# Kernel tuning notes

Hardware: AMD Instinct MI355X
Metric: run time of the kernel (lower is better)

Reference implementation:

```python
import jax, jax.numpy as jnp
import numpy as np

B, N, DIM = 4, 16384, 512
H, D, S = 8, 64, 64  # heads, dim_head, n_global_queries
SCALE = 1.0  # FLARE hardcodes scale=1.0


def setup_inputs() -> dict:
    key = jax.random.key(0)
    ks = jax.random.split(key, 10)
    inner = H * D
    s = 0.02
    return {
        "x": jax.random.normal(ks[0], (B, N, DIM), dtype=jnp.float32),
        "q_global": jax.random.normal(ks[1], (1, H, S, D), dtype=jnp.float32),
        "Wx": jax.random.normal(ks[2], (DIM, inner), dtype=jnp.float32) * s,
        "bx": jnp.zeros((inner,), dtype=jnp.float32),
        "Wk": jax.random.normal(ks[3], (D, D), dtype=jnp.float32) * s,
        "bk": jnp.zeros((D,), dtype=jnp.float32),
        "Wv": jax.random.normal(ks[4], (D, D), dtype=jnp.float32) * s,
        "bv": jnp.zeros((D,), dtype=jnp.float32),
        "Wo": jax.random.normal(ks[5], (inner, DIM), dtype=jnp.float32) * s,
        "bo": jnp.zeros((DIM,), dtype=jnp.float32),
    }


def reference(x, q_global, Wx, bx, Wk, bk, Wv, bv, Wo, bo):
    b, n, c = x.shape
    # input projection + split heads: B N (H D) -> B H N D
    x_mid = (x @ Wx + bx).reshape(b, n, H, D).transpose(0, 2, 1, 3)
    # per-head k/v projections (dim_head x dim_head)
    k = x_mid @ Wk + bk  # [B,H,N,D]
    v = x_mid @ Wv + bv  # [B,H,N,D]
    G = q_global  # broadcast over batch
    # pass 1: aggregate tokens into S global slots
    attn1 = jax.nn.softmax(jnp.einsum('bhsd,bhnd->bhsn', jnp.broadcast_to(G, (b, H, S, D)), k) * SCALE, axis=-1)
    z = jnp.einsum('bhsn,bhnd->bhsd', attn1, v)  # [B,H,S,D]
    # pass 2: distribute slots back to tokens (query=k, key=G, value=z)
    attn2 = jax.nn.softmax(jnp.einsum('bhnd,bhsd->bhns', k, jnp.broadcast_to(G, (b, H, S, D))) * SCALE, axis=-1)
    y = jnp.einsum('bhns,bhsd->bhnd', attn2, z)  # [B,H,N,D]
    # merge heads + output projection
    out = y.transpose(0, 2, 1, 3).reshape(b, n, H * D)
    return out @ Wo + bo
```

## Files before the change

kernel.cpp:

```cpp
#include <hip/hip_runtime.h>
#include <stdint.h>

#define DEV __device__ __forceinline__

typedef __attribute__((ext_vector_type(8))) short bf16x8;
typedef __attribute__((ext_vector_type(4))) float f32x4;
typedef __attribute__((ext_vector_type(8))) unsigned short u16x8;
typedef __attribute__((ext_vector_type(4))) unsigned short u16x4;

DEV unsigned short f2bf(float f) {
  union { float f; unsigned int u; } v; v.f = f;
  unsigned int u = v.u;
  return (unsigned short)((u + 0x7FFFu + ((u >> 16) & 1u)) >> 16);
}

DEV f32x4 mfma16(bf16x8 a, bf16x8 b, f32x4 c) {
  return __builtin_amdgcn_mfma_f32_16x16x32_bf16(a, b, c, 0, 0, 0);
}

DEV void gl_lds16(const void* g, void* l) {
  __builtin_amdgcn_global_load_lds(
      (const __attribute__((address_space(1))) void*)g,
      (__attribute__((address_space(3))) void*)l, 16, 0, 0);
}

__global__ __launch_bounds__(256) void k_cvt_bf16(const float* __restrict__ in,
                                                  unsigned short* __restrict__ out,
                                                  int n8) {
  int i = blockIdx.x * 256 + threadIdx.x;
  if (i >= n8) return;
  const float4* p = (const float4*)in + (size_t)i * 2;
  float4 a = p[0], b = p[1];
  u16x8 o;
  o[0] = f2bf(a.x); o[1] = f2bf(a.y); o[2] = f2bf(a.z); o[3] = f2bf(a.w);
  o[4] = f2bf(b.x); o[5] = f2bf(b.y); o[6] = f2bf(b.z); o[7] = f2bf(b.w);
  ((u16x8*)out)[i] = o;
}

__global__ __launch_bounds__(256) void k_fuse_wkv(const float* __restrict__ Wx,
                                                  const float* __restrict__ Wk,
                                                  const float* __restrict__ Wv,
                                                  unsigned short* __restrict__ WkvT) {
  int idx = blockIdx.x * 256 + threadIdx.x;
  int o = idx >> 9;
  int c = idx & 511;
  const float* W = (o < 512) ? Wk : Wv;
  int oo = o & 511;
  int hb = oo & ~63;
  int dp = oo & 63;
  float s = 0.f;
#pragma unroll 8
  for (int d = 0; d < 64; ++d) s += Wx[(size_t)c * 512 + hb + d] * W[d * 64 + dp];
  WkvT[(size_t)o * 512 + c] = f2bf(s);
}

__global__ void k_fuse_bias(const float* __restrict__ bx, const float* __restrict__ bk,
                            const float* __restrict__ bv, const float* __restrict__ Wk,
                            const float* __restrict__ Wv, float* __restrict__ bkv) {
  int o = blockIdx.x * 256 + threadIdx.x;
  if (o >= 1024) return;
  const float* W = (o < 512) ? Wk : Wv;
  const float* bb = (o < 512) ? bk : bv;
  int oo = o & 511, hb = oo & ~63, dp = oo & 63;
  float s = bb[dp];
  for (int d = 0; d < 64; ++d) s += bx[hb + d] * W[d * 64 + dp];
  bkv[o] = s;
}

__global__ void k_wo_t(const float* __restrict__ Wo, unsigned short* __restrict__ WoT) {
  int idx = blockIdx.x * 256 + threadIdx.x;
  int i = idx >> 9, o = idx & 511;
  WoT[(size_t)o * 512 + i] = f2bf(Wo[(size_t)i * 512 + o]);
}

template <int MODE>
__global__ __launch_bounds__(256) void k_gemm(const unsigned short* __restrict__ A,
                                              const unsigned short* __restrict__ BT,
                                              const float* __restrict__ bias,
                                              void* __restrict__ Cptr,
                                              unsigned short* __restrict__ vT, int NT) {
  __shared__ unsigned short As[2][128 * 64];
  __shared__ unsigned short Bs[2][128 * 64];
  const int tid = threadIdx.x;
  const int w = tid >> 6, lane = tid & 63;
  const int l = lane & 15, g = lane >> 4;
  unsigned bid = blockIdx.x;
  unsigned perx = gridDim.x >> 3;
  unsigned nbid = (bid & 7) * perx + (bid >> 3);
  const int ntile = nbid % NT, mtile = nbid / NT;
  const int bm = mtile * 128, bn = ntile * 128;
  const int wm = (w >> 1) * 64, wn = (w & 1) * 64;
  const int lr = lane >> 3;
  const int lc = (lane & 7) * 8;
  f32x4 acc[4][4] = {};

#define STAGE(buf, k0)                                                        \
  {                                                                           \
    _Pragma("unroll") for (int i = 0; i < 4; ++i) {                           \
      int q = w * 4 + i;                                                      \
      int row = q * 8 + lr;                                                   \
      gl_lds16(A + (size_t)(bm + row) * 512 + (k0) + lc, &As[buf][q * 512]);  \
      gl_lds16(BT + (size_t)(bn + row) * 512 + (k0) + lc, &Bs[buf][q * 512]); \
    }                                                                         \
  }

  STAGE(0, 0);
  __syncthreads();
  int cur = 0;
#pragma unroll 2
  for (int t = 0; t < 8; ++t) {
    if (t < 7) STAGE(cur ^ 1, (t + 1) * 64);
#pragma unroll
    for (int ks = 0; ks < 2; ++ks) {
      bf16x8 af[4], bfr[4];
#pragma unroll
      for (int fm = 0; fm < 4; ++fm)
        af[fm] = *(const bf16x8*)&As[cur][(wm + fm * 16 + l) * 64 + ks * 32 + g * 8];
#pragma unroll
      for (int fn = 0; fn < 4; ++fn)
        bfr[fn] = *(const bf16x8*)&Bs[cur][(wn + fn * 16 + l) * 64 + ks * 32 + g * 8];
#pragma unroll
      for (int fm = 0; fm < 4; ++fm)
#pragma unroll
        for (int fn = 0; fn < 4; ++fn)
          acc[fm][fn] = mfma16(af[fm], bfr[fn], acc[fm][fn]);
    }
    __syncthreads();
    cur ^= 1;
  }
#undef STAGE

#pragma unroll
  for (int fm = 0; fm < 4; ++fm)
#pragma unroll
    for (int fn = 0; fn < 4; ++fn) {
      int colg = bn + wn + fn * 16 + l;
      float bcol = bias[colg];
      int row0 = bm + wm + fm * 16 + g * 4;
      if (MODE == 0) {
#pragma unroll
        for (int r = 0; r < 4; ++r)
          ((float*)Cptr)[(size_t)(row0 + r) * 512 + colg] = acc[fm][fn][r] + bcol;
      } else {
        if (colg < 512) {
#pragma unroll
          for (int r = 0; r < 4; ++r)
            ((unsigned short*)Cptr)[(size_t)(row0 + r) * 512 + colg] =
                f2bf(acc[fm][fn][r] + bcol);
        } else {
          int c2 = colg - 512, h = c2 >> 6, d = c2 & 63;
          int b = row0 >> 14, nn = row0 & 16383;
          u16x4 o;
#pragma unroll
          for (int r = 0; r < 4; ++r) o[r] = f2bf(acc[fm][fn][r] + bcol);
          *(u16x4*)&vT[(((size_t)(b * 8 + h)) * 64 + d) * 16384 + nn] = o;
        }
      }
    }
}

__global__ __launch_bounds__(256) void k_pass1(const unsigned short* __restrict__ kb,
                                               const unsigned short* __restrict__ vT,
                                               const float* __restrict__ qg,
                                               float* __restrict__ zpart,
                                               float* __restrict__ mpart,
                                               float* __restrict__ dpart) {
  __shared__ unsigned short Gs[64 * 72];
  __shared__ unsigned short Ks[128 * 72];
  __shared__ unsigned short Vs[64 * 136];
  __shared__ unsigned short Ps[64 * 136];
  int chunk = blockIdx.x, bh = blockIdx.y;
  int b = bh >> 3, h = bh & 7;
  int tid = threadIdx.x, w = tid >> 6, lane = tid & 63, l = lane & 15, g = lane >> 4;
  {
    int s = tid >> 2, dc = (tid & 3) * 16;
    const float* src = qg + ((size_t)h * 64 + s) * 64 + dc;
    u16x8 o0, o1;
#pragma unroll
    for (int e = 0; e < 8; ++e) { o0[e] = f2bf(src[e]); o1[e] = f2bf(src[8 + e]); }
    *(u16x8*)&Gs[s * 72 + dc] = o0;
    *(u16x8*)&Gs[s * 72 + dc + 8] = o1;
  }
  f32x4 zacc[4] = {};
  float m_run = -1e30f, d_run = 0.f;
  int n_base = chunk * 1024;
  for (int t = 0; t < 8; ++t) {
    int n0 = n_base + t * 128;
#pragma unroll
    for (int i = 0; i < 4; ++i) {
      int cc = i * 256 + tid;
      int nl = cc >> 3, dc = (cc & 7) * 8;
      *(u16x8*)&Ks[nl * 72 + dc] =
          *(const u16x8*)&kb[((size_t)(b * 16384 + n0 + nl)) * 512 + h * 64 + dc];
    }
#pragma unroll
    for (int i = 0; i < 4; ++i) {
      int cc = i * 256 + tid;
      int d = cc >> 4, nc = (cc & 15) * 8;
      *(u16x8*)&Vs[d * 136 + nc] =
          *(const u16x8*)&vT[((size_t)(bh * 64 + d)) * 16384 + n0 + nc];
    }
    __syncthreads();
    f32x4 sacc[8] = {};
#pragma unroll
    for (int ks = 0; ks < 2; ++ks) {
      bf16x8 bq = *(const bf16x8*)&Gs[(w * 16 + l) * 72 + ks * 32 + g * 8];
#pragma unroll
      for (int fm = 0; fm < 8; ++fm) {
        bf16x8 ak = *(const bf16x8*)&Ks[(fm * 16 + l) * 72 + ks * 32 + g * 8];
        sacc[fm] = mfma16(ak, bq, sacc[fm]);
      }
    }
    float tmax = -1e30f;
#pragma unroll
    for (int fm = 0; fm < 8; ++fm)
#pragma unroll
      for (int r = 0; r < 4; ++r) tmax = fmaxf(tmax, sacc[fm][r]);
    tmax = fmaxf(tmax, __shfl_xor(tmax, 16));
    tmax = fmaxf(tmax, __shfl_xor(tmax, 32));
    float newm = fmaxf(m_run, tmax);
    float scale = __expf(m_run - newm);
    float psum = 0.f;
#pragma unroll
    for (int fm = 0; fm < 8; ++fm) {
      u16x4 pp;
#pragma unroll
      for (int r = 0; r < 4; ++r) {
        float p = __expf(sacc[fm][r] - newm);
        psum += p;
        pp[r] = f2bf(p);
      }
      *(u16x4*)&Ps[(w * 16 + l) * 136 + fm * 16 + g * 4] = pp;
    }
    psum += __shfl_xor(psum, 16);
    psum += __shfl_xor(psum, 32);
    d_run = d_run * scale + psum;
    m_run = newm;
    float sc[4];
#pragma unroll
    for (int r = 0; r < 4; ++r) sc[r] = __shfl(scale, g * 4 + r);
#pragma unroll
    for (int fd = 0; fd < 4; ++fd)
#pragma unroll
      for (int r = 0; r < 4; ++r) zacc[fd][r] *= sc[r];
#pragma unroll
    for (int kc = 0; kc < 4; ++kc) {
      bf16x8 ap = *(const bf16x8*)&Ps[(w * 16 + l) * 136 + kc * 32 + g * 8];
#pragma unroll
      for (int fd = 0; fd < 4; ++fd) {
        bf16x8 bv = *(const bf16x8*)&Vs[(fd * 16 + l) * 136 + kc * 32 + g * 8];
        zacc[fd] = mfma16(ap, bv, zacc[fd]);
      }
    }
    __syncthreads();
  }
  size_t base = ((size_t)bh * 16 + chunk) * 64;
#pragma unroll
  for (int fd = 0; fd < 4; ++fd)
#pragma unroll
    for (int r = 0; r < 4; ++r) {
      int s = w * 16 + g * 4 + r, d = fd * 16 + l;
      zpart[(base + s) * 64 + d] = zacc[fd][r];
    }
  if (g == 0) {
    mpart[base + w * 16 + l] = m_run;
    dpart[base + w * 16 + l] = d_run;
  }
}

__global__ void k_zred(const float* __restrict__ zpart, const float* __restrict__ mpart,
                       const float* __restrict__ dpart, unsigned short* __restrict__ zT) {
  int bh = blockIdx.x, tid = threadIdx.x;
  for (int i = 0; i < 16; ++i) {
    int idx = i * 256 + tid;
    int s = idx >> 6, d = idx & 63;
    float mg = -1e30f;
    for (int c = 0; c < 16; ++c) mg = fmaxf(mg, mpart[((size_t)bh * 16 + c) * 64 + s]);
    float den = 0.f, num = 0.f;
    for (int c = 0; c < 16; ++c) {
      float e = __expf(mpart[((size_t)bh * 16 + c) * 64 + s] - mg);
      den += e * dpart[((size_t)bh * 16 + c) * 64 + s];
      num += e * zpart[(((size_t)bh * 16 + c) * 64 + s) * 64 + d];
    }
    zT[((size_t)bh * 64 + d) * 64 + s] = f2bf(num / den);
  }
}

__global__ __launch_bounds__(256) void k_pass2(const unsigned short* __restrict__ kb,
                                               const unsigned short* __restrict__ zT,
                                               const float* __restrict__ qg,
                                               unsigned short* __restrict__ y) {
  __shared__ unsigned short Gs[64 * 72];
  __shared__ unsigned short Zs[64 * 72];
  __shared__ unsigned short P2s[4][32 * 72];
  int tc = blockIdx.x, bh = blockIdx.y, b = bh >> 3, h = bh & 7;
  int tid = threadIdx.x, w = tid >> 6, lane = tid & 63, l = lane & 15, g = lane >> 4;
  {
    int s = tid >> 2, dc = (tid & 3) * 16;
    const float* src = qg + ((size_t)h * 64 + s) * 64 + dc;
    u16x8 o0, o1;
#pragma unroll
    for (int e = 0; e < 8; ++e) { o0[e] = f2bf(src[e]); o1[e] = f2bf(src[8 + e]); }
    *(u16x8*)&Gs[s * 72 + dc] = o0;
    *(u16x8*)&Gs[s * 72 + dc + 8] = o1;
#pragma unroll
    for (int j = 0; j < 2; ++j) {
      int cc = j * 256 + tid;
      int d2 = cc >> 3, sc8 = (cc & 7) * 8;
      *(u16x8*)&Zs[d2 * 72 + sc8] = *(const u16x8*)&zT[((size_t)bh * 64 + d2) * 64 + sc8];
    }
  }
  __syncthreads();
  for (int it = 0; it < 4; ++it) {
    int tok0 = tc * 512 + w * 128 + it * 32;
    bf16x8 ak[2][2];
#pragma unroll
    for (int fm = 0; fm < 2; ++fm)
#pragma unroll
      for (int ks = 0; ks < 2; ++ks)
        ak[fm][ks] = *(const bf16x8*)&kb[((size_t)(b * 16384) + tok0 + fm * 16 + l) * 512 +
                                         h * 64 + ks * 32 + g * 8];
    f32x4 sacc[2][4] = {};
#pragma unroll
    for (int ks = 0; ks < 2; ++ks)
#pragma unroll
      for (int fs = 0; fs < 4; ++fs) {
        bf16x8 bq = *(const bf16x8*)&Gs[(fs * 16 + l) * 72 + ks * 32 + g * 8];
#pragma unroll
        for (int fm = 0; fm < 2; ++fm) sacc[fm][fs] = mfma16(ak[fm][ks], bq, sacc[fm][fs]);
      }
    float inv_[2][4];
#pragma unroll
    for (int fm = 0; fm < 2; ++fm) {
      float mx[4];
#pragma unroll
      for (int r = 0; r < 4; ++r) {
        float m4 = fmaxf(fmaxf(sacc[fm][0][r], sacc[fm][1][r]),
                         fmaxf(sacc[fm][2][r], sacc[fm][3][r]));
#pragma unroll
        for (int msk = 1; msk < 16; msk <<= 1) m4 = fmaxf(m4, __shfl_xor(m4, msk));
        mx[r] = m4;
      }
#pragma unroll
      for (int r = 0; r < 4; ++r) {
        float s4 = 0.f;
#pragma unroll
        for (int fs = 0; fs < 4; ++fs) {
          float p = __expf(sacc[fm][fs][r] - mx[r]);
          sacc[fm][fs][r] = p;
          s4 += p;
        }
#pragma unroll
        for (int msk = 1; msk < 16; msk <<= 1) s4 += __shfl_xor(s4, msk);
        inv_[fm][r] = 1.f / s4;
      }
#pragma unroll
      for (int fs = 0; fs < 4; ++fs)
#pragma unroll
        for (int r = 0; r < 4; ++r)
          P2s[w][(fm * 16 + g * 4 + r) * 72 + fs * 16 + l] = f2bf(sacc[fm][fs][r]);
    }
    f32x4 yacc[2][4] = {};
#pragma unroll
    for (int kc = 0; kc < 2; ++kc) {
      bf16x8 aP[2];
#pragma unroll
      for (int fm = 0; fm < 2; ++fm)
        aP[fm] = *(const bf16x8*)&P2s[w][(fm * 16 + l) * 72 + kc * 32 + g * 8];
#pragma unroll
      for (int fd = 0; fd < 4; ++fd) {
        bf16x8 bz = *(const bf16x8*)&Zs[(fd * 16 + l) * 72 + kc * 32 + g * 8];
#pragma unroll
        for (int fm = 0; fm < 2; ++fm) yacc[fm][fd] = mfma16(aP[fm], bz, yacc[fm][fd]);
      }
    }
#pragma unroll
    for (int fm = 0; fm < 2; ++fm)
#pragma unroll
      for (int fd = 0; fd < 4; ++fd)
#pragma unroll
        for (int r = 0; r < 4; ++r) {
          int tok = tok0 + fm * 16 + g * 4 + r;
          y[((size_t)(b * 16384) + tok) * 512 + h * 64 + fd * 16 + l] =
              f2bf(yacc[fm][fd][r] * inv_[fm][r]);
        }
  }
}

extern "C" void kernel_launch(void* const* d_in, const int* in_sizes, int n_in,
                              void* d_out, int out_size, void* d_ws, size_t ws_size,
                              hipStream_t stream) {
  const float* x  = (const float*)d_in[0];
  const float* qg = (const float*)d_in[1];
  const float* Wx = (const float*)d_in[2];
  const float* bx = (const float*)d_in[3];
  const float* Wk = (const float*)d_in[4];
  const float* bk = (const float*)d_in[5];
  const float* Wv = (const float*)d_in[6];
  const float* bv = (const float*)d_in[7];
  const float* Wo = (const float*)d_in[8];
  const float* bo = (const float*)d_in[9];
  float* out = (float*)d_out;

  char* ws = (char*)d_ws;
  unsigned short* xbf  = (unsigned short*)(ws);
  unsigned short* vT   = (unsigned short*)(ws + 67108864);
  unsigned short* WkvT = (unsigned short*)(ws + 134217728);
  unsigned short* WoT  = (unsigned short*)(ws + 135266304);
  float* bkv           = (float*)(ws + 135790592);
  float* zpart         = (float*)(ws + 135794688);
  float* mpart         = (float*)(ws + 144183296);
  float* dpart         = (float*)(ws + 144314368);
  unsigned short* zT   = (unsigned short*)(ws + 144445440);
  unsigned short* kbuf = (unsigned short*)d_out;

  k_cvt_bf16<<<dim3(16384), dim3(256), 0, stream>>>(x, xbf, 4194304);
  k_fuse_wkv<<<dim3(2048), dim3(256), 0, stream>>>(Wx, Wk, Wv, WkvT);
  k_fuse_bias<<<dim3(4), dim3(256), 0, stream>>>(bx, bk, bv, Wk, Wv, bkv);
  k_wo_t<<<dim3(1024), dim3(256), 0, stream>>>(Wo, WoT);
  k_gemm<1><<<dim3(4096), dim3(256), 0, stream>>>(xbf, WkvT, bkv, (void*)kbuf, vT, 8);
  k_pass1<<<dim3(16, 32), dim3(256), 0, stream>>>(kbuf, vT, qg, zpart, mpart, dpart);
  k_zred<<<dim3(32), dim3(256), 0, stream>>>(zpart, mpart, dpart, zT);
  k_pass2<<<dim3(32, 32), dim3(256), 0, stream>>>(kbuf, zT, qg, xbf);
  k_gemm<0><<<dim3(2048), dim3(256), 0, stream>>>(xbf, WoT, bo, (void*)out, nullptr, 4);
}
```

Measured before the change: 327.3 us.

## Fold global queries into projection weights and fold z into output projection

Precomputes Wx·Wk·Gᵀ so the first GEMM emits attention logits L directly instead of k, which removes the QK matmuls from both passes. Pass 2 and the output projection merge into one GEMM: a per-row softmax of L times a per-batch z·Wo matrix. The first GEMM's K-tile shrinks from 64 to 32, and pass1 now reads V straight from global memory rather than staging it in LDS. In exchange it adds several small precompute kernels, rounds the logits to bf16, and writes a per-batch zWoT matrix.

```diff
diff --git a/kernel.cpp b/kernel.cpp
--- a/kernel.cpp
+++ b/kernel.cpp
@@ -13,11 +13,13 @@
   unsigned int u = v.u;
   return (unsigned short)((u + 0x7FFFu + ((u >> 16) & 1u)) >> 16);
 }
-
+DEV float bf2f(unsigned short u) {
+  union { unsigned int u; float f; } v; v.u = ((unsigned int)u) << 16;
+  return v.f;
+}
 DEV f32x4 mfma16(bf16x8 a, bf16x8 b, f32x4 c) {
   return __builtin_amdgcn_mfma_f32_16x16x32_bf16(a, b, c, 0, 0, 0);
 }
-
 DEV void gl_lds16(const void* g, void* l) {
   __builtin_amdgcn_global_load_lds(
       (const __attribute__((address_space(1))) void*)g,
@@ -37,34 +39,59 @@
   ((u16x8*)out)[i] = o;
 }
 
-__global__ __launch_bounds__(256) void k_fuse_wkv(const float* __restrict__ Wx,
-                                                  const float* __restrict__ Wk,
-                                                  const float* __restrict__ Wv,
-                                                  unsigned short* __restrict__ WkvT) {
+__global__ void k_gk(const float* __restrict__ Wk, const float* __restrict__ qg,
+                     float* __restrict__ GK) {
   int idx = blockIdx.x * 256 + threadIdx.x;
-  int o = idx >> 9;
-  int c = idx & 511;
-  const float* W = (o < 512) ? Wk : Wv;
-  int oo = o & 511;
-  int hb = oo & ~63;
-  int dp = oo & 63;
-  float s = 0.f;
+  int dd = idx & 63, s = (idx >> 6) & 63, h = idx >> 12;
+  float a = 0.f;
 #pragma unroll 8
-  for (int d = 0; d < 64; ++d) s += Wx[(size_t)c * 512 + hb + d] * W[d * 64 + dp];
-  WkvT[(size_t)o * 512 + c] = f2bf(s);
-}
-
-__global__ void k_fuse_bias(const float* __restrict__ bx, const float* __restrict__ bk,
-                            const float* __restrict__ bv, const float* __restrict__ Wk,
-                            const float* __restrict__ Wv, float* __restrict__ bkv) {
+  for (int d = 0; d < 64; ++d) a += Wk[dd * 64 + d] * qg[((size_t)(h * 64 + s)) * 64 + d];
+  GK[idx] = a;
+}
+
+__global__ void k_wl(const float* __restrict__ Wx, const float* __restrict__ GK,
+                     unsigned short* __restrict__ Wcat) {
+  int idx = blockIdx.x * 256 + threadIdx.x;
+  int c = idx & 511, hs = idx >> 9;
+  int h = hs >> 6;
+  float a = 0.f;
+#pragma unroll 8
+  for (int dd = 0; dd < 64; ++dd) a += Wx[(size_t)c * 512 + h * 64 + dd] * GK[hs * 64 + dd];
+  Wcat[(size_t)hs * 512 + c] = f2bf(a);
+}
+
+__global__ void k_wv(const float* __restrict__ Wx, const float* __restrict__ Wv,
+                     unsigned short* __restrict__ Wcat) {
+  int idx = blockIdx.x * 256 + threadIdx.x;
+  int c = idx & 511, o = idx >> 9;
+  int h = o >> 6, dp = o & 63;
+  float a = 0.f;
+#pragma unroll 8
+  for (int dd = 0; dd < 64; ++dd) a += Wx[(size_t)c * 512 + h * 64 + dd] * Wv[dd * 64 + dp];
+  Wcat[(size_t)(512 + o) * 512 + c] = f2bf(a);
+}
+
+__global__ void k_bias(const float* __restrict__ bx, const float* __restrict__ bk,
+                       const float* __restrict__ bv, const float* __restrict__ Wk,
+                       const float* __restrict__ Wv, const float* __restrict__ qg,
+                       float* __restrict__ bias) {
   int o = blockIdx.x * 256 + threadIdx.x;
   if (o >= 1024) return;
-  const float* W = (o < 512) ? Wk : Wv;
-  const float* bb = (o < 512) ? bk : bv;
-  int oo = o & 511, hb = oo & ~63, dp = oo & 63;
-  float s = bb[dp];
-  for (int d = 0; d < 64; ++d) s += bx[hb + d] * W[d * 64 + dp];
-  bkv[o] = s;
+  if (o < 512) {
+    int h = o >> 6, s = o & 63;
+    float a = 0.f;
+    for (int dp = 0; dp < 64; ++dp) {
+      float bkf = bk[dp];
+      for (int dd = 0; dd < 64; ++dd) bkf += bx[h * 64 + dd] * Wk[dd * 64 + dp];
+      a += bkf * qg[((size_t)(h * 64 + s)) * 64 + dp];
+    }
+    bias[o] = a;
+  } else {
+    int o2 = o - 512, h = o2 >> 6, dp = o2 & 63;
+    float a = bv[dp];
+    for (int dd = 0; dd < 64; ++dd) a += bx[h * 64 + dd] * Wv[dd * 64 + dp];
+    bias[o] = a;
+  }
 }
 
 __global__ void k_wo_t(const float* __restrict__ Wo, unsigned short* __restrict__ WoT) {
@@ -73,14 +100,13 @@
   WoT[(size_t)o * 512 + i] = f2bf(Wo[(size_t)i * 512 + o]);
 }
 
-template <int MODE>
-__global__ __launch_bounds__(256) void k_gemm(const unsigned short* __restrict__ A,
-                                              const unsigned short* __restrict__ BT,
-                                              const float* __restrict__ bias,
-                                              void* __restrict__ Cptr,
-                                              unsigned short* __restrict__ vT, int NT) {
-  __shared__ unsigned short As[2][128 * 64];
-  __shared__ unsigned short Bs[2][128 * 64];
+__global__ __launch_bounds__(256) void k_gemm1(const unsigned short* __restrict__ A,
+                                               const unsigned short* __restrict__ BT,
+                                               const float* __restrict__ bias,
+                                               unsigned short* __restrict__ Lout,
+                                               unsigned short* __restrict__ vT, int NT) {
+  __shared__ unsigned short As[2][4096];
+  __shared__ unsigned short Bs[2][4096];
   const int tid = threadIdx.x;
   const int w = tid >> 6, lane = tid & 63;
   const int l = lane & 15, g = lane >> 4;
@@ -90,45 +116,42 @@
   const int ntile = nbid % NT, mtile = nbid / NT;
   const int bm = mtile * 128, bn = ntile * 128;
   const int wm = (w >> 1) * 64, wn = (w & 1) * 64;
-  const int lr = lane >> 3;
-  const int lc = (lane & 7) * 8;
+  const int lr = lane >> 2;
+  const int lc = (lane & 3) * 8;
   f32x4 acc[4][4] = {};
 
-#define STAGE(buf, k0)                                                        \
+#define STG(buf, k0)                                                          \
   {                                                                           \
-    _Pragma("unroll") for (int i = 0; i < 4; ++i) {                           \
-      int q = w * 4 + i;                                                      \
-      int row = q * 8 + lr;                                                   \
+    _Pragma("unroll") for (int i = 0; i < 2; ++i) {                           \
+      int q = w * 2 + i;                                                      \
+      int row = q * 16 + lr;                                                  \
       gl_lds16(A + (size_t)(bm + row) * 512 + (k0) + lc, &As[buf][q * 512]);  \
       gl_lds16(BT + (size_t)(bn + row) * 512 + (k0) + lc, &Bs[buf][q * 512]); \
     }                                                                         \
   }
 
-  STAGE(0, 0);
+  STG(0, 0);
   __syncthreads();
   int cur = 0;
 #pragma unroll 2
-  for (int t = 0; t < 8; ++t) {
-    if (t < 7) STAGE(cur ^ 1, (t + 1) * 64);
-#pragma unroll
-    for (int ks = 0; ks < 2; ++ks) {
-      bf16x8 af[4], bfr[4];
-#pragma unroll
-      for (int fm = 0; fm < 4; ++fm)
-        af[fm] = *(const bf16x8*)&As[cur][(wm + fm * 16 + l) * 64 + ks * 32 + g * 8];
+  for (int t = 0; t < 16; ++t) {
+    if (t < 15) STG(cur ^ 1, (t + 1) * 32);
+    bf16x8 af[4], bfr[4];
+#pragma unroll
+    for (int fm = 0; fm < 4; ++fm)
+      af[fm] = *(const bf16x8*)&As[cur][(wm + fm * 16 + l) * 32 + g * 8];
+#pragma unroll
+    for (int fn = 0; fn < 4; ++fn)
+      bfr[fn] = *(const bf16x8*)&Bs[cur][(wn + fn * 16 + l) * 32 + g * 8];
+#pragma unroll
+    for (int fm = 0; fm < 4; ++fm)
 #pragma unroll
       for (int fn = 0; fn < 4; ++fn)
-        bfr[fn] = *(const bf16x8*)&Bs[cur][(wn + fn * 16 + l) * 64 + ks * 32 + g * 8];
-#pragma unroll
-      for (int fm = 0; fm < 4; ++fm)
-#pragma unroll
-        for (int fn = 0; fn < 4; ++fn)
-          acc[fm][fn] = mfma16(af[fm], bfr[fn], acc[fm][fn]);
-    }
+        acc[fm][fn] = mfma16(af[fm], bfr[fn], acc[fm][fn]);
     __syncthreads();
     cur ^= 1;
   }
-#undef STAGE
+#undef STG
 
 #pragma unroll
   for (int fm = 0; fm < 4; ++fm)
@@ -137,101 +160,74 @@
       int colg = bn + wn + fn * 16 + l;
       float bcol = bias[colg];
       int row0 = bm + wm + fm * 16 + g * 4;
-      if (MODE == 0) {
+      if (colg < 512) {
 #pragma unroll
         for (int r = 0; r < 4; ++r)
-          ((float*)Cptr)[(size_t)(row0 + r) * 512 + colg] = acc[fm][fn][r] + bcol;
+          Lout[(size_t)(row0 + r) * 512 + colg] = f2bf(acc[fm][fn][r] + bcol);
       } else {
-        if (colg < 512) {
-#pragma unroll
-          for (int r = 0; r < 4; ++r)
-            ((unsigned short*)Cptr)[(size_t)(row0 + r) * 512 + colg] =
-                f2bf(acc[fm][fn][r] + bcol);
-        } else {
-          int c2 = colg - 512, h = c2 >> 6, d = c2 & 63;
-          int b = row0 >> 14, nn = row0 & 16383;
-          u16x4 o;
-#pragma unroll
-          for (int r = 0; r < 4; ++r) o[r] = f2bf(acc[fm][fn][r] + bcol);
-          *(u16x4*)&vT[(((size_t)(b * 8 + h)) * 64 + d) * 16384 + nn] = o;
-        }
-      }
-    }
-}
-
-__global__ __launch_bounds__(256) void k_pass1(const unsigned short* __restrict__ kb,
+        int c2 = colg - 512, h = c2 >> 6, d = c2 & 63;
+        int b = row0 >> 14, nn = row0 & 16383;
+        u16x4 o;
+#pragma unroll
+        for (int r = 0; r < 4; ++r) o[r] = f2bf(acc[fm][fn][r] + bcol);
+        *(u16x4*)&vT[(((size_t)(b * 8 + h)) * 64 + d) * 16384 + nn] = o;
+      }
+    }
+}
+
+__global__ __launch_bounds__(256) void k_pass1(const unsigned short* __restrict__ L,
                                                const unsigned short* __restrict__ vT,
-                                               const float* __restrict__ qg,
                                                float* __restrict__ zpart,
                                                float* __restrict__ mpart,
                                                float* __restrict__ dpart) {
-  __shared__ unsigned short Gs[64 * 72];
-  __shared__ unsigned short Ks[128 * 72];
-  __shared__ unsigned short Vs[64 * 136];
-  __shared__ unsigned short Ps[64 * 136];
+  __shared__ unsigned short Ls[64 * 128];
   int chunk = blockIdx.x, bh = blockIdx.y;
   int b = bh >> 3, h = bh & 7;
   int tid = threadIdx.x, w = tid >> 6, lane = tid & 63, l = lane & 15, g = lane >> 4;
-  {
-    int s = tid >> 2, dc = (tid & 3) * 16;
-    const float* src = qg + ((size_t)h * 64 + s) * 64 + dc;
-    u16x8 o0, o1;
-#pragma unroll
-    for (int e = 0; e < 8; ++e) { o0[e] = f2bf(src[e]); o1[e] = f2bf(src[8 + e]); }
-    *(u16x8*)&Gs[s * 72 + dc] = o0;
-    *(u16x8*)&Gs[s * 72 + dc + 8] = o1;
-  }
+  const int sn = tid & 127, sg = tid >> 7;
   f32x4 zacc[4] = {};
   float m_run = -1e30f, d_run = 0.f;
-  int n_base = chunk * 1024;
+  const int s = w * 16 + l;
   for (int t = 0; t < 8; ++t) {
-    int n0 = n_base + t * 128;
-#pragma unroll
-    for (int i = 0; i < 4; ++i) {
-      int cc = i * 256 + tid;
-      int nl = cc >> 3, dc = (cc & 7) * 8;
-      *(u16x8*)&Ks[nl * 72 + dc] =
-          *(const u16x8*)&kb[((size_t)(b * 16384 + n0 + nl)) * 512 + h * 64 + dc];
-    }
-#pragma unroll
-    for (int i = 0; i < 4; ++i) {
-      int cc = i * 256 + tid;
-      int d = cc >> 4, nc = (cc & 15) * 8;
-      *(u16x8*)&Vs[d * 136 + nc] =
-          *(const u16x8*)&vT[((size_t)(bh * 64 + d)) * 16384 + n0 + nc];
+    int n0 = chunk * 1024 + t * 128;
+    if (t) __syncthreads();
+#pragma unroll
+    for (int j = 0; j < 4; ++j) {
+      int s0 = sg * 32 + j * 8;
+      u16x8 vl = *(const u16x8*)&L[((size_t)(b * 16384 + n0 + sn)) * 512 + h * 64 + s0];
+#pragma unroll
+      for (int e = 0; e < 8; ++e) {
+        int ss = s0 + e;
+        Ls[(ss * 256 + ((sn * 2) ^ ((ss & 7) << 4))) >> 1] = vl[e];
+      }
     }
     __syncthreads();
-    f32x4 sacc[8] = {};
-#pragma unroll
-    for (int ks = 0; ks < 2; ++ks) {
-      bf16x8 bq = *(const bf16x8*)&Gs[(w * 16 + l) * 72 + ks * 32 + g * 8];
-#pragma unroll
-      for (int fm = 0; fm < 8; ++fm) {
-        bf16x8 ak = *(const bf16x8*)&Ks[(fm * 16 + l) * 72 + ks * 32 + g * 8];
-        sacc[fm] = mfma16(ak, bq, sacc[fm]);
-      }
-    }
+    bf16x8 aL[4];
+#pragma unroll
+    for (int kc = 0; kc < 4; ++kc)
+      aL[kc] = *(const bf16x8*)&Ls[(s * 256 + ((kc * 64 + g * 16) ^ ((s & 7) << 4))) >> 1];
+    float fv[32];
+#pragma unroll
+    for (int kc = 0; kc < 4; ++kc)
+#pragma unroll
+      for (int e = 0; e < 8; ++e) fv[kc * 8 + e] = bf2f((unsigned short)aL[kc][e]);
     float tmax = -1e30f;
 #pragma unroll
-    for (int fm = 0; fm < 8; ++fm)
-#pragma unroll
-      for (int r = 0; r < 4; ++r) tmax = fmaxf(tmax, sacc[fm][r]);
+    for (int i = 0; i < 32; ++i) tmax = fmaxf(tmax, fv[i]);
     tmax = fmaxf(tmax, __shfl_xor(tmax, 16));
     tmax = fmaxf(tmax, __shfl_xor(tmax, 32));
     float newm = fmaxf(m_run, tmax);
     float scale = __expf(m_run - newm);
     float psum = 0.f;
-#pragma unroll
-    for (int fm = 0; fm < 8; ++fm) {
-      u16x4 pp;
-#pragma unroll
-      for (int r = 0; r < 4; ++r) {
-        float p = __expf(sacc[fm][r] - newm);
+    bf16x8 pf[4];
+#pragma unroll
+    for (int kc = 0; kc < 4; ++kc)
+#pragma unroll
+      for (int e = 0; e < 8; ++e) {
+        float p = __expf(fv[kc * 8 + e] - newm);
         psum += p;
-        pp[r] = f2bf(p);
-      }
-      *(u16x4*)&Ps[(w * 16 + l) * 136 + fm * 16 + g * 4] = pp;
-    }
+        pf[kc][e] = (short)f2bf(p);
+      }
     psum += __shfl_xor(psum, 16);
     psum += __shfl_xor(psum, 32);
     d_run = d_run * scale + psum;
@@ -245,22 +241,21 @@
       for (int r = 0; r < 4; ++r) zacc[fd][r] *= sc[r];
 #pragma unroll
     for (int kc = 0; kc < 4; ++kc) {
-      bf16x8 ap = *(const bf16x8*)&Ps[(w * 16 + l) * 136 + kc * 32 + g * 8];
 #pragma unroll
       for (int fd = 0; fd < 4; ++fd) {
-        bf16x8 bv = *(const bf16x8*)&Vs[(fd * 16 + l) * 136 + kc * 32 + g * 8];
-        zacc[fd] = mfma16(ap, bv, zacc[fd]);
-      }
-    }
-    __syncthreads();
+        bf16x8 bv = *(const bf16x8*)&vT[((size_t)(bh * 64 + fd * 16 + l)) * 16384 + n0 +
+                                        kc * 32 + g * 8];
+        zacc[fd] = mfma16(pf[kc], bv, zacc[fd]);
+      }
+    }
   }
   size_t base = ((size_t)bh * 16 + chunk) * 64;
 #pragma unroll
   for (int fd = 0; fd < 4; ++fd)
 #pragma unroll
     for (int r = 0; r < 4; ++r) {
-      int s = w * 16 + g * 4 + r, d = fd * 16 + l;
-      zpart[(base + s) * 64 + d] = zacc[fd][r];
+      int so = w * 16 + g * 4 + r, d = fd * 16 + l;
+      zpart[(base + so) * 64 + d] = zacc[fd][r];
     }
   if (g == 0) {
     mpart[base + w * 16 + l] = m_run;
@@ -269,7 +264,7 @@
 }
 
 __global__ void k_zred(const float* __restrict__ zpart, const float* __restrict__ mpart,
-                       const float* __restrict__ dpart, unsigned short* __restrict__ zT) {
+                       const float* __restrict__ dpart, float* __restrict__ z) {
   int bh = blockIdx.x, tid = threadIdx.x;
   for (int i = 0; i < 16; ++i) {
     int idx = i * 256 + tid;
@@ -282,108 +277,94 @@
       den += e * dpart[((size_t)bh * 16 + c) * 64 + s];
       num += e * zpart[(((size_t)bh * 16 + c) * 64 + s) * 64 + d];
     }
-    zT[((size_t)bh * 64 + d) * 64 + s] = f2bf(num / den);
-  }
-}
-
-__global__ __launch_bounds__(256) void k_pass2(const unsigned short* __restrict__ kb,
-                                               const unsigned short* __restrict__ zT,
-                                               const float* __restrict__ qg,
-                                               unsigned short* __restrict__ y) {
-  __shared__ unsigned short Gs[64 * 72];
-  __shared__ unsigned short Zs[64 * 72];
-  __shared__ unsigned short P2s[4][32 * 72];
-  int tc = blockIdx.x, bh = blockIdx.y, b = bh >> 3, h = bh & 7;
+    z[(size_t)bh * 4096 + idx] = num / den;
+  }
+}
+
+__global__ void k_zwo(const float* __restrict__ z, const unsigned short* __restrict__ WoT,
+                      unsigned short* __restrict__ zWoT) {
+  int idx = blockIdx.x * 256 + threadIdx.x;
+  int hs = idx & 511, c = (idx >> 9) & 511, b = idx >> 18;
+  int h = hs >> 6, s = hs & 63;
+  const float* zp = z + ((size_t)(b * 8 + h) * 64 + s) * 64;
+  const unsigned short* wp = WoT + (size_t)c * 512 + h * 64;
+  float a = 0.f;
+#pragma unroll 8
+  for (int d = 0; d < 64; ++d) a += zp[d] * bf2f(wp[d]);
+  zWoT[((size_t)(b * 512) + c) * 512 + hs] = f2bf(a);
+}
+
+__global__ __launch_bounds__(256) void k_gemm2(const unsigned short* __restrict__ L,
+                                               const unsigned short* __restrict__ zWoT,
+                                               const float* __restrict__ bo,
+                                               float* __restrict__ out) {
+  __shared__ unsigned short P2s[64 * 520];
+  int row0 = blockIdx.x * 64;
+  int b = row0 >> 14;
   int tid = threadIdx.x, w = tid >> 6, lane = tid & 63, l = lane & 15, g = lane >> 4;
   {
-    int s = tid >> 2, dc = (tid & 3) * 16;
-    const float* src = qg + ((size_t)h * 64 + s) * 64 + dc;
-    u16x8 o0, o1;
-#pragma unroll
-    for (int e = 0; e < 8; ++e) { o0[e] = f2bf(src[e]); o1[e] = f2bf(src[8 + e]); }
-    *(u16x8*)&Gs[s * 72 + dc] = o0;
-    *(u16x8*)&Gs[s * 72 + dc + 8] = o1;
-#pragma unroll
-    for (int j = 0; j < 2; ++j) {
-      int cc = j * 256 + tid;
-      int d2 = cc >> 3, sc8 = (cc & 7) * 8;
-      *(u16x8*)&Zs[d2 * 72 + sc8] = *(const u16x8*)&zT[((size_t)bh * 64 + d2) * 64 + sc8];
+    int row = tid >> 2, q = tid & 3;
+    const unsigned short* lp = L + (size_t)(row0 + row) * 512;
+#pragma unroll
+    for (int hh = 0; hh < 2; ++hh) {
+      int h = q * 2 + hh;
+      float f[64];
+#pragma unroll
+      for (int j = 0; j < 8; ++j) {
+        u16x8 rv = *(const u16x8*)&lp[h * 64 + j * 8];
+#pragma unroll
+        for (int e = 0; e < 8; ++e) f[j * 8 + e] = bf2f(rv[e]);
+      }
+      float mx = -1e30f;
+#pragma unroll
+      for (int i = 0; i < 64; ++i) mx = fmaxf(mx, f[i]);
+      float sm = 0.f;
+#pragma unroll
+      for (int i = 0; i < 64; ++i) {
+        float p = __expf(f[i] - mx);
+        f[i] = p;
+        sm += p;
+      }
+      float inv = 1.f / sm;
+#pragma unroll
+      for (int j = 0; j < 8; ++j) {
+        u16x8 o;
+#pragma unroll
+        for (int e = 0; e < 8; ++e) o[e] = f2bf(f[j * 8 + e] * inv);
+        *(u16x8*)((char*)P2s + (row * 1040 + h * 128 + j * 16)) = o;
+      }
     }
   }
   __syncthreads();
-  for (int it = 0; it < 4; ++it) {
-    int tok0 = tc * 512 + w * 128 + it * 32;
-    bf16x8 ak[2][2];
-#pragma unroll
-    for (int fm = 0; fm < 2; ++fm)
-#pragma unroll
-      for (int ks = 0; ks < 2; ++ks)
-        ak[fm][ks] = *(const bf16x8*)&kb[((size_t)(b * 16384) + tok0 + fm * 16 + l) * 512 +
-                                         h * 64 + ks * 32 + g * 8];
-    f32x4 sacc[2][4] = {};
-#pragma unroll
-    for (int ks = 0; ks < 2; ++ks)
-#pragma unroll
-      for (int fs = 0; fs < 4; ++fs) {
-        bf16x8 bq = *(const bf16x8*)&Gs[(fs * 16 + l) * 72 + ks * 32 + g * 8];
-#pragma unroll
-        for (int fm = 0; fm < 2; ++fm) sacc[fm][fs] = mfma16(ak[fm][ks], bq, sacc[fm][fs]);
-      }
-    float inv_[2][4];
-#pragma unroll
-    for (int fm = 0; fm < 2; ++fm) {
-      float mx[4];
-#pragma unroll
-      for (int r = 0; r < 4; ++r) {
-        float m4 = fmaxf(fmaxf(sacc[fm][0][r], sacc[fm][1][r]),
-                         fmaxf(sacc[fm][2][r], sacc[fm][3][r]));
-#pragma unroll
-        for (int msk = 1; msk < 16; msk <<= 1) m4 = fmaxf(m4, __shfl_xor(m4, msk));
-        mx[r] = m4;
-      }
-#pragma unroll
-      for (int r = 0; r < 4; ++r) {
-        float s4 = 0.f;
-#pragma unroll
-        for (int fs = 0; fs < 4; ++fs) {
-          float p = __expf(sacc[fm][fs][r] - mx[r]);
-          sacc[fm][fs][r] = p;
-          s4 += p;
-        }
-#pragma unroll
-        for (int msk = 1; msk < 16; msk <<= 1) s4 += __shfl_xor(s4, msk);
-        inv_[fm][r] = 1.f / s4;
-      }
-#pragma unroll
-      for (int fs = 0; fs < 4; ++fs)
+#pragma unroll
+  for (int p = 0; p < 2; ++p) {
+    f32x4 acc[4][4] = {};
+#pragma unroll 4
+    for (int kc = 0; kc < 16; ++kc) {
+      bf16x8 aA[4], bB[4];
+#pragma unroll
+      for (int fm = 0; fm < 4; ++fm)
+        aA[fm] = *(const bf16x8*)((const char*)P2s + ((fm * 16 + l) * 1040 + kc * 64 + g * 16));
+#pragma unroll
+      for (int fn = 0; fn < 4; ++fn) {
+        int col = w * 128 + p * 64 + fn * 16 + l;
+        bB[fn] = *(const bf16x8*)&zWoT[((size_t)(b * 512) + col) * 512 + kc * 32 + g * 8];
+      }
+#pragma unroll
+      for (int fm = 0; fm < 4; ++fm)
+#pragma unroll
+        for (int fn = 0; fn < 4; ++fn) acc[fm][fn] = mfma16(aA[fm], bB[fn], acc[fm][fn]);
+    }
+#pragma unroll
+    for (int fm = 0; fm < 4; ++fm)
+#pragma unroll
+      for (int fn = 0; fn < 4; ++fn) {
+        int col = w * 128 + p * 64 + fn * 16 + l;
+        float bb = bo[col];
 #pragma unroll
         for (int r = 0; r < 4; ++r)
-          P2s[w][(fm * 16 + g * 4 + r) * 72 + fs * 16 + l] = f2bf(sacc[fm][fs][r]);
-    }
-    f32x4 yacc[2][4] = {};
-#pragma unroll
-    for (int kc = 0; kc < 2; ++kc) {
-      bf16x8 aP[2];
-#pragma unroll
-      for (int fm = 0; fm < 2; ++fm)
-        aP[fm] = *(const bf16x8*)&P2s[w][(fm * 16 + l) * 72 + kc * 32 + g * 8];
-#pragma unroll
-      for (int fd = 0; fd < 4; ++fd) {
-        bf16x8 bz = *(const bf16x8*)&Zs[(fd * 16 + l) * 72 + kc * 32 + g * 8];
-#pragma unroll
-        for (int fm = 0; fm < 2; ++fm) yacc[fm][fd] = mfma16(aP[fm], bz, yacc[fm][fd]);
-      }
-    }
-#pragma unroll
-    for (int fm = 0; fm < 2; ++fm)
-#pragma unroll
-      for (int fd = 0; fd < 4; ++fd)
-#pragma unroll
-        for (int r = 0; r < 4; ++r) {
-          int tok = tok0 + fm * 16 + g * 4 + r;
-          y[((size_t)(b * 16384) + tok) * 512 + h * 64 + fd * 16 + l] =
-              f2bf(yacc[fm][fd][r] * inv_[fm][r]);
-        }
+          out[(size_t)(row0 + fm * 16 + g * 4 + r) * 512 + col] = acc[fm][fn][r] + bb;
+      }
   }
 }
 
@@ -404,23 +385,28 @@
 
   char* ws = (char*)d_ws;
   unsigned short* xbf  = (unsigned short*)(ws);
-  unsigned short* vT   = (unsigned short*)(ws + 67108864);
-  unsigned short* WkvT = (unsigned short*)(ws + 134217728);
+  unsigned short* Lbuf = (unsigned short*)(ws + 67108864);
+  unsigned short* Wcat = (unsigned short*)(ws + 134217728);
   unsigned short* WoT  = (unsigned short*)(ws + 135266304);
-  float* bkv           = (float*)(ws + 135790592);
-  float* zpart         = (float*)(ws + 135794688);
-  float* mpart         = (float*)(ws + 144183296);
-  float* dpart         = (float*)(ws + 144314368);
-  unsigned short* zT   = (unsigned short*)(ws + 144445440);
-  unsigned short* kbuf = (unsigned short*)d_out;
+  float* bias          = (float*)(ws + 135790592);
+  float* GK            = (float*)(ws + 135794688);
+  unsigned short* zWoT = (unsigned short*)(ws + 135925760);
+  char* dout = (char*)d_out;
+  unsigned short* vT = (unsigned short*)(dout);
+  float* zpart       = (float*)(dout + 67108864);
+  float* mpart       = (float*)(dout + 75497472);
+  float* dpart       = (float*)(dout + 75628544);
+  float* zbuf        = (float*)(dout + 75759616);
 
   k_cvt_bf16<<<dim3(16384), dim3(256), 0, stream>>>(x, xbf, 4194304);
-  k_fuse_wkv<<<dim3(2048), dim3(256), 0, stream>>>(Wx, Wk, Wv, WkvT);
-  k_fuse_bias<<<dim3(4), dim3(256), 0, stream>>>(bx, bk, bv, Wk, Wv, bkv);
+  k_gk<<<dim3(128), dim3(256), 0, stream>>>(Wk, qg, GK);
+  k_wl<<<dim3(1024), dim3(256), 0, stream>>>(Wx, GK, Wcat);
+  k_wv<<<dim3(1024), dim3(256), 0, stream>>>(Wx, Wv, Wcat);
+  k_bias<<<dim3(4), dim3(256), 0, stream>>>(bx, bk, bv, Wk, Wv, qg, bias);
   k_wo_t<<<dim3(1024), dim3(256), 0, stream>>>(Wo, WoT);
-  k_gemm<1><<<dim3(4096), dim3(256), 0, stream>>>(xbf, WkvT, bkv, (void*)kbuf, vT, 8);
-  k_pass1<<<dim3(16, 32), dim3(256), 0, stream>>>(kbuf, vT, qg, zpart, mpart, dpart);
-  k_zred<<<dim3(32), dim3(256), 0, stream>>>(zpart, mpart, dpart, zT);
-  k_pass2<<<dim3(32, 32), dim3(256), 0, stream>>>(kbuf, zT, qg, xbf);
-  k_gemm<0><<<dim3(2048), dim3(256), 0, stream>>>(xbf, WoT, bo, (void*)out, nullptr, 4);
-}
+  k_gemm1<<<dim3(4096), dim3(256), 0, stream>>>(xbf, Wcat, bias, Lbuf, vT, 8);
+  k_pass1<<<dim3(16, 32), dim3(256), 0, stream>>>(Lbuf, vT, zpart, mpart, dpart);
+  k_zred<<<dim3(32), dim3(256), 0, stream>>>(zpart, mpart, dpart, zbuf);
+  k_zwo<<<dim3(4096), dim3(256), 0, stream>>>(zbuf, WoT, zWoT);
+  k_gemm2<<<dim3(1024), dim3(256), 0, stream>>>(Lbuf, zWoT, bo, out);
+}
```

Result: slower. 428.3 us (+30.9%).
